# Kernel tuning notes

Hardware: AMD Instinct MI355X
Metric: run time of the kernel (lower is better)

## Reference

```python
import jax, jax.numpy as jnp
import numpy as np

ALPHA = 10.0   # cfg.alpha (VolSDF density scale)
BETA = 0.05    # cfg.beta  (Laplace CDF scale)
EPS = 1e-10
FAR_DELTA = 1e10  # delta appended for last sample
NEAR, FAR = 2.0, 6.0


def setup_inputs() -> dict:
    key = jax.random.key(0)
    k1, k2, k3 = jax.random.split(key, 3)
    N, d = 65536, 128
    signed_distance = jax.random.normal(k1, (N, d), dtype=jnp.float32)
    color = jax.random.uniform(k2, (N, d, 3), dtype=jnp.float32)
    # monotonically increasing sample depths along each ray in [NEAR, FAR]
    depth_values = NEAR + (FAR - NEAR) * jnp.sort(
        jax.random.uniform(k3, (N, d), dtype=jnp.float32), axis=-1)
    return {"signed_distance": signed_distance, "color": color,
            "depth_values": depth_values}


def sdf_to_density(sd, alpha, beta):
    # density = alpha * LaplaceCDF(-sd); cdf(s) = 0.5 exp(s/b) if s<=0 else 1-0.5 exp(-s/b)
    s = -sd
    return alpha * jnp.where(s <= 0, 0.5 * jnp.exp(s / beta),
                             1.0 - 0.5 * jnp.exp(-s / beta))


def reference(signed_distance, color, depth_values):
    # deltas: [N, d], last delta = 1e10 (opaque background)
    deltas = jnp.concatenate(
        [depth_values[:, 1:] - depth_values[:, :-1],
         jnp.full_like(depth_values[:, :1], FAR_DELTA)], axis=-1)
    density = sdf_to_density(signed_distance, ALPHA, BETA)  # [N, d]
    # log of per-step transmittance factor: -sigma*delta + eps (eps kept to match torch)
    t = -density * deltas + EPS                              # [N, d]
    # T_i = prod_{j<i} exp(t_j) = exp(exclusive cumsum of t)
    log_T = jnp.concatenate(
        [jnp.zeros_like(t[:, :1]), jnp.cumsum(t[:, :-1], axis=-1)], axis=-1)
    weights = jnp.exp(log_T) * (1.0 - jnp.exp(t))            # [N, d]
    out_color = jnp.einsum('nd,ndc->nc', weights, color)     # [N, 3]
    return out_color
```

## Files before the change

kernel.cpp:

```cpp
#include <hip/hip_runtime.h>

#define ALPHA_C   10.0f
#define INV_BETA  20.0f
#define EPS_C     1e-10f
#define FAR_DELTA 1e10f

__global__ __launch_bounds__(256) void volsdf_render_kernel(
    const float* __restrict__ sd,
    const float* __restrict__ color,
    const float* __restrict__ depth,
    float* __restrict__ out,
    int N)
{
    const int wave = (int)((blockIdx.x * blockDim.x + threadIdx.x) >> 6);
    const int lane = (int)(threadIdx.x & 63);
    if (wave >= N) return;

    const size_t base = (size_t)wave * 128 + (size_t)lane * 2;

    const float2 sd2 = *reinterpret_cast<const float2*>(sd + base);
    const float2 dp2 = *reinterpret_cast<const float2*>(depth + base);
    const float* cb  = color + (size_t)wave * 384 + (size_t)lane * 6;
    const float2 c01 = *reinterpret_cast<const float2*>(cb + 0);
    const float2 c23 = *reinterpret_cast<const float2*>(cb + 2);
    const float2 c45 = *reinterpret_cast<const float2*>(cb + 4);

    const float dnext  = __shfl_down(dp2.x, 1, 64);
    const float delta0 = dp2.y - dp2.x;
    const float delta1 = (lane == 63) ? FAR_DELTA : (dnext - dp2.y);

    const float s0 = -sd2.x, s1 = -sd2.y;
    const float e0 = __expf(-fabsf(s0) * INV_BETA);
    const float e1 = __expf(-fabsf(s1) * INV_BETA);
    const float den0 = ALPHA_C * ((s0 <= 0.0f) ? 0.5f * e0 : 1.0f - 0.5f * e0);
    const float den1 = ALPHA_C * ((s1 <= 0.0f) ? 0.5f * e1 : 1.0f - 0.5f * e1);

    const float t0 = -den0 * delta0 + EPS_C;
    const float t1 = -den1 * delta1 + EPS_C;

    const float tl = t0 + t1;
    float incl = tl;
    #pragma unroll
    for (int off = 1; off < 64; off <<= 1) {
        const float up = __shfl_up(incl, off, 64);
        if (lane >= off) incl += up;
    }
    float excl = __shfl_up(incl, 1, 64);
    if (lane == 0) excl = 0.0f;

    const float w0 = __expf(excl)      * (1.0f - __expf(t0));
    const float w1 = __expf(excl + t0) * (1.0f - __expf(t1));

    float accr = w0 * c01.x + w1 * c23.y;
    float accg = w0 * c01.y + w1 * c45.x;
    float accb = w0 * c23.x + w1 * c45.y;

    #pragma unroll
    for (int off = 32; off >= 1; off >>= 1) {
        accr += __shfl_xor(accr, off, 64);
        accg += __shfl_xor(accg, off, 64);
        accb += __shfl_xor(accb, off, 64);
    }

    if (lane == 0) {
        float* o = out + (size_t)wave * 3;
        o[0] = accr;
        o[1] = accg;
        o[2] = accb;
    }
}

extern "C" void kernel_launch(void* const* d_in, const int* in_sizes, int n_in,
                              void* d_out, int out_size, void* d_ws, size_t ws_size,
                              hipStream_t stream) {
    const float* sd    = (const float*)d_in[0];
    const float* color = (const float*)d_in[1];
    const float* depth = (const float*)d_in[2];
    float* out = (float*)d_out;

    const int N = in_sizes[0] / 128;
    const int block = 256;
    const int grid = (N * 64 + block - 1) / block;
    volsdf_render_kernel<<<grid, block, 0, stream>>>(sd, color, depth, out, N);
}
```

Measured before the change: 29.24 us.

## Process two rays per wave with four samples per lane and float4 loads

```diff
diff --git a/kernel.cpp b/kernel.cpp
--- a/kernel.cpp
+++ b/kernel.cpp
@@ -12,58 +12,80 @@
     float* __restrict__ out,
     int N)
 {
-    const int wave = (int)((blockIdx.x * blockDim.x + threadIdx.x) >> 6);
+    const int tid  = (int)(blockIdx.x * blockDim.x + threadIdx.x);
+    const int wave = tid >> 6;
     const int lane = (int)(threadIdx.x & 63);
-    if (wave >= N) return;
+    const int half = lane >> 5;
+    const int gl   = lane & 31;
+    const int ray  = wave * 2 + half;
+    if (ray >= N) return;
 
-    const size_t base = (size_t)wave * 128 + (size_t)lane * 2;
+    const size_t rbase = (size_t)ray * 128 + (size_t)gl * 4;
+    const float4 sd4 = *reinterpret_cast<const float4*>(sd + rbase);
+    const float4 dp4 = *reinterpret_cast<const float4*>(depth + rbase);
+    const float* cb  = color + (size_t)ray * 384 + (size_t)gl * 12;
+    const float4 f0 = *reinterpret_cast<const float4*>(cb + 0);
+    const float4 f1 = *reinterpret_cast<const float4*>(cb + 4);
+    const float4 f2 = *reinterpret_cast<const float4*>(cb + 8);
 
-    const float2 sd2 = *reinterpret_cast<const float2*>(sd + base);
-    const float2 dp2 = *reinterpret_cast<const float2*>(depth + base);
-    const float* cb  = color + (size_t)wave * 384 + (size_t)lane * 6;
-    const float2 c01 = *reinterpret_cast<const float2*>(cb + 0);
-    const float2 c23 = *reinterpret_cast<const float2*>(cb + 2);
-    const float2 c45 = *reinterpret_cast<const float2*>(cb + 4);
+    const float dnext  = __shfl_down(dp4.x, 1, 32);
+    const float delta0 = dp4.y - dp4.x;
+    const float delta1 = dp4.z - dp4.y;
+    const float delta2 = dp4.w - dp4.z;
+    const float delta3 = (gl == 31) ? FAR_DELTA : (dnext - dp4.w);
 
-    const float dnext  = __shfl_down(dp2.x, 1, 64);
-    const float delta0 = dp2.y - dp2.x;
-    const float delta1 = (lane == 63) ? FAR_DELTA : (dnext - dp2.y);
-
-    const float s0 = -sd2.x, s1 = -sd2.y;
+    const float s0 = -sd4.x, s1 = -sd4.y, s2 = -sd4.z, s3 = -sd4.w;
     const float e0 = __expf(-fabsf(s0) * INV_BETA);
     const float e1 = __expf(-fabsf(s1) * INV_BETA);
+    const float e2 = __expf(-fabsf(s2) * INV_BETA);
+    const float e3 = __expf(-fabsf(s3) * INV_BETA);
     const float den0 = ALPHA_C * ((s0 <= 0.0f) ? 0.5f * e0 : 1.0f - 0.5f * e0);
     const float den1 = ALPHA_C * ((s1 <= 0.0f) ? 0.5f * e1 : 1.0f - 0.5f * e1);
+    const float den2 = ALPHA_C * ((s2 <= 0.0f) ? 0.5f * e2 : 1.0f - 0.5f * e2);
+    const float den3 = ALPHA_C * ((s3 <= 0.0f) ? 0.5f * e3 : 1.0f - 0.5f * e3);
 
     const float t0 = -den0 * delta0 + EPS_C;
     const float t1 = -den1 * delta1 + EPS_C;
+    const float t2 = -den2 * delta2 + EPS_C;
+    const float t3 = -den3 * delta3 + EPS_C;
 
-    const float tl = t0 + t1;
+    const float p1 = t0;
+    const float p2 = t0 + t1;
+    const float p3 = p2 + t2;
+    const float tl = p3 + t3;
     float incl = tl;
     #pragma unroll
-    for (int off = 1; off < 64; off <<= 1) {
-        const float up = __shfl_up(incl, off, 64);
-        if (lane >= off) incl += up;
+    for (int off = 1; off < 32; off <<= 1) {
+        const float up = __shfl_up(incl, off, 32);
+        if (gl >= off) incl += up;
     }
-    float excl = __shfl_up(incl, 1, 64);
-    if (lane == 0) excl = 0.0f;
+    float excl = __shfl_up(incl, 1, 32);
+    if (gl == 0) excl = 0.0f;
 
-    const float w0 = __expf(excl)      * (1.0f - __expf(t0));
-    const float w1 = __expf(excl + t0) * (1.0f - __expf(t1));
+    const float T0  = __expf(excl);
+    const float et0 = __expf(t0), et1 = __expf(t1);
+    const float et2 = __expf(t2), et3 = __expf(t3);
+    const float T1 = T0 * et0;
+    const float T2 = T1 * et1;
+    const float T3 = T2 * et2;
+    const float w0 = T0 * (1.0f - et0);
+    const float w1 = T1 * (1.0f - et1);
+    const float w2 = T2 * (1.0f - et2);
+    const float w3 = T3 * (1.0f - et3);
 
-    float accr = w0 * c01.x + w1 * c23.y;
-    float accg = w0 * c01.y + w1 * c45.x;
-    float accb = w0 * c23.x + w1 * c45.y;
+    float accr = w0 * f0.x + w1 * f0.w + w2 * f1.z + w3 * f2.y;
+    float accg = w0 * f0.y + w1 * f1.x + w2 * f1.w + w3 * f2.z;
+    float accb = w0 * f0.z + w1 * f1.y + w2 * f2.x + w3 * f2.w;
 
     #pragma unroll
-    for (int off = 32; off >= 1; off >>= 1) {
-        accr += __shfl_xor(accr, off, 64);
-        accg += __shfl_xor(accg, off, 64);
-        accb += __shfl_xor(accb, off, 64);
+    for (int off = 16; off >= 1; off >>= 1) {
+        accr += __shfl_xor(accr, off, 32);
+        accg += __shfl_xor(accg, off, 32);
+        accb += __shfl_xor(accb, off, 32);
     }
 
-    if (lane == 0) {
-        float* o = out + (size_t)wave * 3;
+    if (gl == 0) {
+        float* o = out + (size_t)ray * 3;
         o[0] = accr;
         o[1] = accg;
         o[2] = accb;
@@ -79,7 +101,8 @@
     float* out = (float*)d_out;
 
     const int N = in_sizes[0] / 128;
+    const int nWaves = (N + 1) / 2;
     const int block = 256;
-    const int grid = (N * 64 + block - 1) / block;
+    const int grid = (nWaves * 64 + block - 1) / block;
     volsdf_render_kernel<<<grid, block, 0, stream>>>(sd, color, depth, out, N);
 }
```

After: 29.11 us. No clear change (-0.4%).

## Process four rays per wave with 8 samples per lane and 16-lane scans

Applied to the files above, without the earlier changes.

```diff
diff --git a/kernel.cpp b/kernel.cpp
--- a/kernel.cpp
+++ b/kernel.cpp
@@ -12,58 +12,89 @@
     float* __restrict__ out,
     int N)
 {
-    const int wave = (int)((blockIdx.x * blockDim.x + threadIdx.x) >> 6);
+    const int tid  = (int)(blockIdx.x * blockDim.x + threadIdx.x);
+    const int wave = tid >> 6;
     const int lane = (int)(threadIdx.x & 63);
-    if (wave >= N) return;
+    const int g    = lane >> 4;
+    const int gl   = lane & 15;
+    const int ray  = wave * 4 + g;
+    if (ray >= N) return;
 
-    const size_t base = (size_t)wave * 128 + (size_t)lane * 2;
+    const size_t rbase = (size_t)ray * 128 + (size_t)gl * 8;
+    const float4 sdA = *reinterpret_cast<const float4*>(sd + rbase);
+    const float4 sdB = *reinterpret_cast<const float4*>(sd + rbase + 4);
+    const float4 dpA = *reinterpret_cast<const float4*>(depth + rbase);
+    const float4 dpB = *reinterpret_cast<const float4*>(depth + rbase + 4);
+    const float* cb  = color + (size_t)ray * 384 + (size_t)gl * 24;
+    const float4 f0 = *reinterpret_cast<const float4*>(cb + 0);
+    const float4 f1 = *reinterpret_cast<const float4*>(cb + 4);
+    const float4 f2 = *reinterpret_cast<const float4*>(cb + 8);
+    const float4 f3 = *reinterpret_cast<const float4*>(cb + 12);
+    const float4 f4 = *reinterpret_cast<const float4*>(cb + 16);
+    const float4 f5 = *reinterpret_cast<const float4*>(cb + 20);
 
-    const float2 sd2 = *reinterpret_cast<const float2*>(sd + base);
-    const float2 dp2 = *reinterpret_cast<const float2*>(depth + base);
-    const float* cb  = color + (size_t)wave * 384 + (size_t)lane * 6;
-    const float2 c01 = *reinterpret_cast<const float2*>(cb + 0);
-    const float2 c23 = *reinterpret_cast<const float2*>(cb + 2);
-    const float2 c45 = *reinterpret_cast<const float2*>(cb + 4);
+    const float dnext = __shfl_down(dpA.x, 1, 16);
+    float dlt[8];
+    dlt[0] = dpA.y - dpA.x;
+    dlt[1] = dpA.z - dpA.y;
+    dlt[2] = dpA.w - dpA.z;
+    dlt[3] = dpB.x - dpA.w;
+    dlt[4] = dpB.y - dpB.x;
+    dlt[5] = dpB.z - dpB.y;
+    dlt[6] = dpB.w - dpB.z;
+    dlt[7] = (gl == 15) ? FAR_DELTA : (dnext - dpB.w);
 
-    const float dnext  = __shfl_down(dp2.x, 1, 64);
-    const float delta0 = dp2.y - dp2.x;
-    const float delta1 = (lane == 63) ? FAR_DELTA : (dnext - dp2.y);
+    const float sdv[8] = {sdA.x, sdA.y, sdA.z, sdA.w, sdB.x, sdB.y, sdB.z, sdB.w};
 
-    const float s0 = -sd2.x, s1 = -sd2.y;
-    const float e0 = __expf(-fabsf(s0) * INV_BETA);
-    const float e1 = __expf(-fabsf(s1) * INV_BETA);
-    const float den0 = ALPHA_C * ((s0 <= 0.0f) ? 0.5f * e0 : 1.0f - 0.5f * e0);
-    const float den1 = ALPHA_C * ((s1 <= 0.0f) ? 0.5f * e1 : 1.0f - 0.5f * e1);
+    float t[8];
+    #pragma unroll
+    for (int i = 0; i < 8; ++i) {
+        const float s = -sdv[i];
+        const float e = __expf(-fabsf(s) * INV_BETA);
+        const float den = ALPHA_C * ((s <= 0.0f) ? 0.5f * e : 1.0f - 0.5f * e);
+        t[i] = -den * dlt[i] + EPS_C;
+    }
 
-    const float t0 = -den0 * delta0 + EPS_C;
-    const float t1 = -den1 * delta1 + EPS_C;
+    float c[8];
+    c[0] = 0.0f;
+    #pragma unroll
+    for (int i = 1; i < 8; ++i) c[i] = c[i - 1] + t[i - 1];
+    const float tl = c[7] + t[7];
 
-    const float tl = t0 + t1;
     float incl = tl;
     #pragma unroll
-    for (int off = 1; off < 64; off <<= 1) {
-        const float up = __shfl_up(incl, off, 64);
-        if (lane >= off) incl += up;
+    for (int off = 1; off < 16; off <<= 1) {
+        const float up = __shfl_up(incl, off, 16);
+        if (gl >= off) incl += up;
     }
-    float excl = __shfl_up(incl, 1, 64);
-    if (lane == 0) excl = 0.0f;
+    float excl = __shfl_up(incl, 1, 16);
+    if (gl == 0) excl = 0.0f;
 
-    const float w0 = __expf(excl)      * (1.0f - __expf(t0));
-    const float w1 = __expf(excl + t0) * (1.0f - __expf(t1));
+    float T = __expf(excl);
+    float w[8];
+    #pragma unroll
+    for (int i = 0; i < 8; ++i) {
+        const float et = __expf(t[i]);
+        w[i] = T * (1.0f - et);
+        T *= et;
+    }
 
-    float accr = w0 * c01.x + w1 * c23.y;
-    float accg = w0 * c01.y + w1 * c45.x;
-    float accb = w0 * c23.x + w1 * c45.y;
+    float accr = w[0]*f0.x + w[1]*f0.w + w[2]*f1.z + w[3]*f2.y
+               + w[4]*f3.x + w[5]*f3.w + w[6]*f4.z + w[7]*f5.y;
+    float accg = w[0]*f0.y + w[1]*f1.x + w[2]*f1.w + w[3]*f2.z
+               + w[4]*f3.y + w[5]*f4.x + w[6]*f4.w + w[7]*f5.z;
+    float accb = w[0]*f0.z + w[1]*f1.y + w[2]*f2.x + w[3]*f2.w
+               + w[4]*f3.z + w[5]*f4.y + w[6]*f5.x + w[7]*f5.w;
 
     #pragma unroll
-    for (int off = 32; off >= 1; off >>= 1) {
-        accr += __shfl_xor(accr, off, 64);
-        accg += __shfl_xor(accg, off, 64);
-        accb += __shfl_xor(accb, off, 64);
+    for (int off = 8; off >= 1; off >>= 1) {
+        accr += __shfl_xor(accr, off, 16);
+        accg += __shfl_xor(accg, off, 16);
+        accb += __shfl_xor(accb, off, 16);
     }
 
-    if (lane == 0) {
-        float* o = out + (size_t)wave * 3;
+    if (gl == 0) {
+        float* o = out + (size_t)ray * 3;
         o[0] = accr;
         o[1] = accg;
         o[2] = accb;
@@ -79,7 +110,8 @@
     float* out = (float*)d_out;
 
     const int N = in_sizes[0] / 128;
+    const int nWaves = (N + 3) / 4;
     const int block = 256;
-    const int grid = (N * 64 + block - 1) / block;
+    const int grid = (nWaves * 64 + block - 1) / block;
     volsdf_render_kernel<<<grid, block, 0, stream>>>(sd, color, depth, out, N);
 }
```

Result: no change. 28.96 us (-0.9%).
